# Performance work log

Measured on AMD Instinct MI355X. Metric: run time of the kernel, lower is better.

## Reference

```python
import jax, jax.numpy as jnp
import numpy as np

N = 100_000        # nodes
E = 3_200_000      # edges (avg degree 32)
F_IN = 2000        # highly-variable genes
H = 16             # hidden dim
C = 3              # KMeans clusters / classes


def setup_inputs() -> dict:
    key = jax.random.key(0)
    k1, k2, k3, k4 = jax.random.split(key, 4)
    x = jax.random.normal(k1, (N, F_IN), dtype=jnp.float32)
    edge_index = jax.random.randint(k2, (2, E), 0, N, dtype=jnp.int32)
    W1 = jax.random.normal(k3, (F_IN, H), dtype=jnp.float32) * (1.0 / np.sqrt(F_IN))
    b1 = jnp.zeros((H,), dtype=jnp.float32)
    W2 = jax.random.normal(k4, (H, C), dtype=jnp.float32) * (1.0 / np.sqrt(H))
    b2 = jnp.zeros((C,), dtype=jnp.float32)
    return {"x": x, "edge_index": edge_index, "W1": W1, "b1": b1, "W2": W2, "b2": b2}


def _gcn_conv(x, W, b, src, dst, n):
    """PyG GCNConv: linear -> add self-loops -> sym-normalized scatter-add -> +bias."""
    h = x @ W                                   # [N, F_out]
    loop = jnp.arange(n, dtype=src.dtype)
    src_sl = jnp.concatenate([src, loop])       # [E+N]
    dst_sl = jnp.concatenate([dst, loop])
    deg = jax.ops.segment_sum(jnp.ones(src_sl.shape[0], dtype=h.dtype), dst_sl, num_segments=n)
    dinv = jax.lax.rsqrt(deg)                   # deg >= 1 due to self-loops
    norm = dinv[src_sl] * dinv[dst_sl]          # [E+N]
    msg = h[src_sl] * norm[:, None]             # gather + scale
    out = jax.ops.segment_sum(msg, dst_sl, num_segments=n)  # scatter-add
    return out + b


def reference(x, edge_index, W1, b1, W2, b2):
    src, dst = edge_index[0], edge_index[1]
    n = x.shape[0]
    h = jax.nn.relu(_gcn_conv(x, W1, b1, src, dst, n))
    # F.dropout with training=False is identity (eval mode)
    logits = _gcn_conv(h, W2, b2, src, dst, n)
    return jax.nn.log_softmax(logits, axis=1)
```

## Files before the change

kernel.cpp:

```cpp
#include <hip/hip_runtime.h>
#include <hip/hip_bf16.h>


#define FIN   2000
#define HDIM  16
#define KB    40
#define NCHUNK (FIN / KB)
#define KSTRIDE 65

__global__ void zero_k(int4* __restrict__ p, int n4) {
    int i = blockIdx.x * 256 + threadIdx.x;
    if (i < n4) p[i] = make_int4(0, 0, 0, 0);
}

__global__ void count_k(const int* __restrict__ dst, int* __restrict__ cnt, int e) {
    int i = (blockIdx.x * 256 + threadIdx.x) * 4;
    if (i + 3 < e) {
        int4 d = *(const int4*)(dst + i);
        atomicAdd(&cnt[d.x], 1);
        atomicAdd(&cnt[d.y], 1);
        atomicAdd(&cnt[d.z], 1);
        atomicAdd(&cnt[d.w], 1);
    } else {
        for (int k = i; k < e; ++k) atomicAdd(&cnt[dst[k]], 1);
    }
}

__global__ __launch_bounds__(1024) void scan_k(const int* __restrict__ cnt,
                                               int* __restrict__ rowptr,
                                               float* __restrict__ dinv, int n) {
    __shared__ int sdata[1024];
    int tid = threadIdx.x;
    int chunk = (n + 1023) >> 10;
    int s0 = tid * chunk;
    int s1 = s0 + chunk; if (s1 > n) s1 = n;
    int sum = 0;
    for (int i = s0; i < s1; ++i) {
        int c = cnt[i];
        dinv[i] = 1.0f / sqrtf((float)(c + 1));
        sum += c;
    }
    sdata[tid] = sum;
    __syncthreads();
    for (int off = 1; off < 1024; off <<= 1) {
        int v = sdata[tid];
        int u = (tid >= off) ? sdata[tid - off] : 0;
        __syncthreads();
        sdata[tid] = v + u;
        __syncthreads();
    }
    int run = sdata[tid] - sum;
    for (int i = s0; i < s1; ++i) { rowptr[i] = run; run += cnt[i]; }
    if (tid == 0) rowptr[n] = sdata[1023];
}

__global__ void scatter_k(const int* __restrict__ src, const int* __restrict__ dst,
                          const int* __restrict__ rowptr, int* __restrict__ cursor,
                          int* __restrict__ col, int e) {
    int i = (blockIdx.x * 256 + threadIdx.x) * 4;
    if (i + 3 < e) {
        int4 d = *(const int4*)(dst + i);
        int4 s = *(const int4*)(src + i);
        col[rowptr[d.x] + atomicAdd(&cursor[d.x], 1)] = s.x;
        col[rowptr[d.y] + atomicAdd(&cursor[d.y], 1)] = s.y;
        col[rowptr[d.z] + atomicAdd(&cursor[d.z], 1)] = s.z;
        col[rowptr[d.w] + atomicAdd(&cursor[d.w], 1)] = s.w;
    } else {
        for (int k = i; k < e; ++k) {
            int d = dst[k];
            col[rowptr[d] + atomicAdd(&cursor[d], 1)] = src[k];
        }
    }
}

__global__ __launch_bounds__(64) void gemm1(const float* __restrict__ x,
                                            const float* __restrict__ W1,
                                            const float* __restrict__ dinv,
                                            float* __restrict__ t1s, int n) {
    __shared__ float xT[2][KB * KSTRIDE];
    const int lane = threadIdx.x;
    const long base = (long)blockIdx.x * 64;

    float4 st[10];

#define STAGE_LOAD(c)                                                       \
    {                                                                       \
        _Pragma("unroll")                                                   \
        for (int i = 0; i < 10; ++i) {                                      \
            int job = i * 64 + lane;                                        \
            int jr = job / 10, jk = job - jr * 10;                          \
            long gr = base + jr; if (gr >= n) gr = n - 1;                   \
            st[i] = *(const float4*)(x + gr * FIN + (c) * KB + jk * 4);     \
        }                                                                   \
    }
#define STAGE_WRITE(bsel)                                                   \
    {                                                                       \
        float* p = &xT[(bsel)][0];                                          \
        _Pragma("unroll")                                                   \
        for (int i = 0; i < 10; ++i) {                                      \
            int job = i * 64 + lane;                                        \
            int jr = job / 10, jk = job - jr * 10;                          \
            p[(jk * 4 + 0) * KSTRIDE + jr] = st[i].x;                       \
            p[(jk * 4 + 1) * KSTRIDE + jr] = st[i].y;                       \
            p[(jk * 4 + 2) * KSTRIDE + jr] = st[i].z;                       \
            p[(jk * 4 + 3) * KSTRIDE + jr] = st[i].w;                       \
        }                                                                   \
    }

    float acc[HDIM];
#pragma unroll
    for (int j = 0; j < HDIM; ++j) acc[j] = 0.0f;

    STAGE_LOAD(0);
    STAGE_WRITE(0);

    for (int c = 0; c < NCHUNK; ++c) {
        int b = c & 1;
        if (c + 1 < NCHUNK) STAGE_LOAD(c + 1);
        const float* w0 = W1 + c * KB * HDIM;
#pragma unroll 4
        for (int k = 0; k < KB; ++k) {
            float xv = xT[b][k * KSTRIDE + lane];
            const float* w = w0 + k * HDIM;
#pragma unroll
            for (int j = 0; j < HDIM; ++j) acc[j] = fmaf(xv, w[j], acc[j]);
        }
        if (c + 1 < NCHUNK) STAGE_WRITE((c + 1) & 1);
    }

    long row = base + lane;
    long rc = row < n ? row : n - 1;
    float s = dinv[rc];
    if (row < n) {
        float4* o = (float4*)(t1s + row * HDIM);
        o[0] = make_float4(acc[0] * s, acc[1] * s, acc[2] * s, acc[3] * s);
        o[1] = make_float4(acc[4] * s, acc[5] * s, acc[6] * s, acc[7] * s);
        o[2] = make_float4(acc[8] * s, acc[9] * s, acc[10] * s, acc[11] * s);
        o[3] = make_float4(acc[12] * s, acc[13] * s, acc[14] * s, acc[15] * s);
    }
#undef STAGE_LOAD
#undef STAGE_WRITE
}

__global__ __launch_bounds__(256) void agg1(const float* __restrict__ t1s,
                                            const int* __restrict__ rowptr,
                                            const int* __restrict__ col,
                                            const float* __restrict__ dinv,
                                            const float* __restrict__ b1,
                                            const float* __restrict__ W2,
                                            float* __restrict__ t2s, int n) {
    int node = blockIdx.x * 4 + (threadIdx.x >> 6);
    if (node >= n) return;
    int lane = threadIdx.x & 63;
    int nb = lane >> 4;
    int j  = lane & 15;
    int e0 = rowptr[node], e1 = rowptr[node + 1];
    float acc = (nb == 0) ? t1s[node * HDIM + j] : 0.0f;
    for (int e = e0 + nb; e < e1; e += 4) {
        acc += t1s[col[e] * HDIM + j];
    }
    acc += __shfl_xor(acc, 16);
    acc += __shfl_xor(acc, 32);
    float dn = dinv[node];
    float h = acc * dn + b1[j];
    h = h > 0.0f ? h : 0.0f;
    float p0 = h * W2[j * 3 + 0];
    float p1 = h * W2[j * 3 + 1];
    float p2 = h * W2[j * 3 + 2];
#pragma unroll
    for (int off = 8; off > 0; off >>= 1) {
        p0 += __shfl_xor(p0, off, 16);
        p1 += __shfl_xor(p1, off, 16);
        p2 += __shfl_xor(p2, off, 16);
    }
    if (lane == 0) {
        *(float4*)(t2s + node * 4) = make_float4(p0 * dn, p1 * dn, p2 * dn, 0.0f);
    }
}

__global__ __launch_bounds__(256) void agg2(const float* __restrict__ t2s,
                                            const int* __restrict__ rowptr,
                                            const int* __restrict__ col,
                                            const float* __restrict__ dinv,
                                            const float* __restrict__ b2,
                                            float* __restrict__ out, int n) {
    int node = blockIdx.x * 256 + threadIdx.x;
    if (node >= n) return;
    float4 a = *(const float4*)(t2s + node * 4);
    float a0 = a.x, a1 = a.y, a2 = a.z;
    int e0 = rowptr[node], e1 = rowptr[node + 1];
#pragma unroll 4
    for (int e = e0; e < e1; ++e) {
        int s = col[e];
        float4 v = *(const float4*)(t2s + s * 4);
        a0 += v.x; a1 += v.y; a2 += v.z;
    }
    float dn = dinv[node];
    float l0 = a0 * dn + b2[0];
    float l1 = a1 * dn + b2[1];
    float l2 = a2 * dn + b2[2];
    float m = fmaxf(l0, fmaxf(l1, l2));
    float lse = logf(expf(l0 - m) + expf(l1 - m) + expf(l2 - m)) + m;
    out[node * 3 + 0] = l0 - lse;
    out[node * 3 + 1] = l1 - lse;
    out[node * 3 + 2] = l2 - lse;
}

extern "C" void kernel_launch(void* const* d_in, const int* in_sizes, int n_in,
                              void* d_out, int out_size, void* d_ws, size_t ws_size,
                              hipStream_t stream) {
    const float* x  = (const float*)d_in[0];
    const int*   ei = (const int*)d_in[1];
    const float* W1 = (const float*)d_in[2];
    const float* b1 = (const float*)d_in[3];
    const float* W2 = (const float*)d_in[4];
    const float* b2 = (const float*)d_in[5];
    const int N = in_sizes[0] / FIN;
    const int E = in_sizes[1] / 2;
    const int* src = ei;
    const int* dst = ei + E;

    char* ws = (char*)d_ws;
    auto alloc = [&](size_t bytes) {
        char* p = ws;
        ws += (bytes + 255) & ~(size_t)255;
        return p;
    };
    size_t npad = ((size_t)N * 4 + 255) & ~(size_t)255;
    int*   cnt    = (int*)alloc(N * 4);
    int*   cursor = (int*)alloc(N * 4);
    int*   rowptr = (int*)alloc((size_t)(N + 1) * 4);
    float* dinv   = (float*)alloc(N * 4);
    int*   col    = (int*)alloc((size_t)E * 4);
    float* t1s    = (float*)alloc((size_t)N * HDIM * 4);
    float* t2s    = (float*)alloc((size_t)N * 4 * 4);

    int n4 = (int)(npad * 2 / 16);
    zero_k<<<(n4 + 255) / 256, 256, 0, stream>>>((int4*)cnt, n4);
    int e4 = (E + 3) / 4;
    count_k<<<(e4 + 255) / 256, 256, 0, stream>>>(dst, cnt, E);
    scan_k<<<1, 1024, 0, stream>>>(cnt, rowptr, dinv, N);
    scatter_k<<<(e4 + 255) / 256, 256, 0, stream>>>(src, dst, rowptr, cursor, col, E);
    gemm1<<<(N + 63) / 64, 64, 0, stream>>>(x, W1, dinv, t1s, N);
    agg1<<<(N + 3) / 4, 256, 0, stream>>>(t1s, rowptr, col, dinv, b1, W2, t2s, N);
    agg2<<<(N + 255) / 256, 256, 0, stream>>>(t2s, rowptr, col, dinv, b2, (float*)d_out, N);
}
```

Before: 857.7 us.

## Co-schedule split GEMM with edge count and CSR scatter in fused launches

The dense x@W1 GEMM is split into two halves. Each half runs in the same launch as one of the atomic-heavy graph-build passes: degree counting, and the CSR column scatter. Because dinv is not yet known when the first GEMM half runs, the GEMM now stores unscaled features, and agg1 multiplies each gathered neighbour row by dinv[src]. agg1 is also remapped to 16 lanes per node with a serial edge loop instead of 4 edge-parallel groups. The aim is to hide the latency-bound atomic passes behind the bandwidth-bound GEMM, at the cost of an extra dinv gather per edge and less edge-level parallelism in aggregation.

Result: no change. 867.3 us (+1.1%).

```diff
diff --git a/kernel.cpp b/kernel.cpp
--- a/kernel.cpp
+++ b/kernel.cpp
@@ -7,22 +7,140 @@
 #define KB    40
 #define NCHUNK (FIN / KB)
 #define KSTRIDE 65
+#define EPB   1024
 
 __global__ void zero_k(int4* __restrict__ p, int n4) {
     int i = blockIdx.x * 256 + threadIdx.x;
     if (i < n4) p[i] = make_int4(0, 0, 0, 0);
 }
 
-__global__ void count_k(const int* __restrict__ dst, int* __restrict__ cnt, int e) {
-    int i = (blockIdx.x * 256 + threadIdx.x) * 4;
-    if (i + 3 < e) {
-        int4 d = *(const int4*)(dst + i);
-        atomicAdd(&cnt[d.x], 1);
-        atomicAdd(&cnt[d.y], 1);
-        atomicAdd(&cnt[d.z], 1);
-        atomicAdd(&cnt[d.w], 1);
+__device__ __forceinline__ void gemm_body(const float* __restrict__ x,
+                                          const float* __restrict__ W1,
+                                          float* __restrict__ t1,
+                                          float xT[2][KB * KSTRIDE],
+                                          long base, int n) {
+    const int lane = threadIdx.x;
+    float4 st[10];
+
+#define STAGE_LOAD(c)                                                       \
+    {                                                                       \
+        _Pragma("unroll")                                                   \
+        for (int i = 0; i < 10; ++i) {                                      \
+            int job = i * 64 + lane;                                        \
+            int jr = job / 10, jk = job - jr * 10;                          \
+            long gr = base + jr; if (gr >= n) gr = n - 1;                   \
+            st[i] = *(const float4*)(x + gr * FIN + (c) * KB + jk * 4);     \
+        }                                                                   \
+    }
+#define STAGE_WRITE(bsel)                                                   \
+    {                                                                       \
+        float* p = &xT[(bsel)][0];                                          \
+        _Pragma("unroll")                                                   \
+        for (int i = 0; i < 10; ++i) {                                      \
+            int job = i * 64 + lane;                                        \
+            int jr = job / 10, jk = job - jr * 10;                          \
+            p[(jk * 4 + 0) * KSTRIDE + jr] = st[i].x;                       \
+            p[(jk * 4 + 1) * KSTRIDE + jr] = st[i].y;                       \
+            p[(jk * 4 + 2) * KSTRIDE + jr] = st[i].z;                       \
+            p[(jk * 4 + 3) * KSTRIDE + jr] = st[i].w;                       \
+        }                                                                   \
+    }
+
+    float acc[HDIM];
+#pragma unroll
+    for (int j = 0; j < HDIM; ++j) acc[j] = 0.0f;
+
+    STAGE_LOAD(0);
+    STAGE_WRITE(0);
+
+    for (int c = 0; c < NCHUNK; ++c) {
+        int b = c & 1;
+        if (c + 1 < NCHUNK) STAGE_LOAD(c + 1);
+        const float* w0 = W1 + c * KB * HDIM;
+        __syncthreads();
+#pragma unroll 4
+        for (int k = 0; k < KB; ++k) {
+            float xv = xT[b][k * KSTRIDE + lane];
+            const float* w = w0 + k * HDIM;
+#pragma unroll
+            for (int j = 0; j < HDIM; ++j) acc[j] = fmaf(xv, w[j], acc[j]);
+        }
+        __syncthreads();
+        if (c + 1 < NCHUNK) STAGE_WRITE((c + 1) & 1);
+    }
+
+    long row = base + lane;
+    if (row < n) {
+        float4* o = (float4*)(t1 + row * HDIM);
+        o[0] = make_float4(acc[0], acc[1], acc[2], acc[3]);
+        o[1] = make_float4(acc[4], acc[5], acc[6], acc[7]);
+        o[2] = make_float4(acc[8], acc[9], acc[10], acc[11]);
+        o[3] = make_float4(acc[12], acc[13], acc[14], acc[15]);
+    }
+#undef STAGE_LOAD
+#undef STAGE_WRITE
+}
+
+__global__ __launch_bounds__(64) void fused_a(const float* __restrict__ x,
+                                              const float* __restrict__ W1,
+                                              float* __restrict__ t1,
+                                              const int* __restrict__ dst,
+                                              int* __restrict__ cnt,
+                                              int n, int e, int ga) {
+    __shared__ float xT[2][KB * KSTRIDE];
+    if ((int)blockIdx.x < ga) {
+        gemm_body(x, W1, t1, xT, (long)blockIdx.x * 64, n);
     } else {
-        for (int k = i; k < e; ++k) atomicAdd(&cnt[dst[k]], 1);
+        int chunk = blockIdx.x - ga;
+        int base = chunk * EPB + (int)threadIdx.x * 4;
+#pragma unroll
+        for (int r = 0; r < 4; ++r) {
+            int i = base + r * 256;
+            if (i + 3 < e) {
+                int4 d = *(const int4*)(dst + i);
+                atomicAdd(&cnt[d.x], 1);
+                atomicAdd(&cnt[d.y], 1);
+                atomicAdd(&cnt[d.z], 1);
+                atomicAdd(&cnt[d.w], 1);
+            } else {
+                for (int k = i; k < e && k < i + 4; ++k) atomicAdd(&cnt[dst[k]], 1);
+            }
+        }
+    }
+}
+
+__global__ __launch_bounds__(64) void fused_b(const float* __restrict__ x,
+                                              const float* __restrict__ W1,
+                                              float* __restrict__ t1,
+                                              const int* __restrict__ src,
+                                              const int* __restrict__ dst,
+                                              const int* __restrict__ rowptr,
+                                              int* __restrict__ cursor,
+                                              int* __restrict__ col,
+                                              int n, int e, int ga, int gb) {
+    __shared__ float xT[2][KB * KSTRIDE];
+    if ((int)blockIdx.x < gb) {
+        gemm_body(x, W1, t1, xT, (long)(ga + blockIdx.x) * 64, n);
+    } else {
+        int chunk = blockIdx.x - gb;
+        int base = chunk * EPB + (int)threadIdx.x * 4;
+#pragma unroll
+        for (int r = 0; r < 4; ++r) {
+            int i = base + r * 256;
+            if (i + 3 < e) {
+                int4 d = *(const int4*)(dst + i);
+                int4 s = *(const int4*)(src + i);
+                col[rowptr[d.x] + atomicAdd(&cursor[d.x], 1)] = s.x;
+                col[rowptr[d.y] + atomicAdd(&cursor[d.y], 1)] = s.y;
+                col[rowptr[d.z] + atomicAdd(&cursor[d.z], 1)] = s.z;
+                col[rowptr[d.w] + atomicAdd(&cursor[d.w], 1)] = s.w;
+            } else {
+                for (int k = i; k < e && k < i + 4; ++k) {
+                    int d = dst[k];
+                    col[rowptr[d] + atomicAdd(&cursor[d], 1)] = src[k];
+                }
+            }
+        }
     }
 }
 
@@ -54,114 +172,24 @@
     if (tid == 0) rowptr[n] = sdata[1023];
 }
 
-__global__ void scatter_k(const int* __restrict__ src, const int* __restrict__ dst,
-                          const int* __restrict__ rowptr, int* __restrict__ cursor,
-                          int* __restrict__ col, int e) {
-    int i = (blockIdx.x * 256 + threadIdx.x) * 4;
-    if (i + 3 < e) {
-        int4 d = *(const int4*)(dst + i);
-        int4 s = *(const int4*)(src + i);
-        col[rowptr[d.x] + atomicAdd(&cursor[d.x], 1)] = s.x;
-        col[rowptr[d.y] + atomicAdd(&cursor[d.y], 1)] = s.y;
-        col[rowptr[d.z] + atomicAdd(&cursor[d.z], 1)] = s.z;
-        col[rowptr[d.w] + atomicAdd(&cursor[d.w], 1)] = s.w;
-    } else {
-        for (int k = i; k < e; ++k) {
-            int d = dst[k];
-            col[rowptr[d] + atomicAdd(&cursor[d], 1)] = src[k];
-        }
-    }
-}
-
-__global__ __launch_bounds__(64) void gemm1(const float* __restrict__ x,
-                                            const float* __restrict__ W1,
-                                            const float* __restrict__ dinv,
-                                            float* __restrict__ t1s, int n) {
-    __shared__ float xT[2][KB * KSTRIDE];
-    const int lane = threadIdx.x;
-    const long base = (long)blockIdx.x * 64;
-
-    float4 st[10];
-
-#define STAGE_LOAD(c)                                                       \
-    {                                                                       \
-        _Pragma("unroll")                                                   \
-        for (int i = 0; i < 10; ++i) {                                      \
-            int job = i * 64 + lane;                                        \
-            int jr = job / 10, jk = job - jr * 10;                          \
-            long gr = base + jr; if (gr >= n) gr = n - 1;                   \
-            st[i] = *(const float4*)(x + gr * FIN + (c) * KB + jk * 4);     \
-        }                                                                   \
-    }
-#define STAGE_WRITE(bsel)                                                   \
-    {                                                                       \
-        float* p = &xT[(bsel)][0];                                          \
-        _Pragma("unroll")                                                   \
-        for (int i = 0; i < 10; ++i) {                                      \
-            int job = i * 64 + lane;                                        \
-            int jr = job / 10, jk = job - jr * 10;                          \
-            p[(jk * 4 + 0) * KSTRIDE + jr] = st[i].x;                       \
-            p[(jk * 4 + 1) * KSTRIDE + jr] = st[i].y;                       \
-            p[(jk * 4 + 2) * KSTRIDE + jr] = st[i].z;                       \
-            p[(jk * 4 + 3) * KSTRIDE + jr] = st[i].w;                       \
-        }                                                                   \
-    }
-
-    float acc[HDIM];
-#pragma unroll
-    for (int j = 0; j < HDIM; ++j) acc[j] = 0.0f;
-
-    STAGE_LOAD(0);
-    STAGE_WRITE(0);
-
-    for (int c = 0; c < NCHUNK; ++c) {
-        int b = c & 1;
-        if (c + 1 < NCHUNK) STAGE_LOAD(c + 1);
-        const float* w0 = W1 + c * KB * HDIM;
-#pragma unroll 4
-        for (int k = 0; k < KB; ++k) {
-            float xv = xT[b][k * KSTRIDE + lane];
-            const float* w = w0 + k * HDIM;
-#pragma unroll
-            for (int j = 0; j < HDIM; ++j) acc[j] = fmaf(xv, w[j], acc[j]);
-        }
-        if (c + 1 < NCHUNK) STAGE_WRITE((c + 1) & 1);
-    }
-
-    long row = base + lane;
-    long rc = row < n ? row : n - 1;
-    float s = dinv[rc];
-    if (row < n) {
-        float4* o = (float4*)(t1s + row * HDIM);
-        o[0] = make_float4(acc[0] * s, acc[1] * s, acc[2] * s, acc[3] * s);
-        o[1] = make_float4(acc[4] * s, acc[5] * s, acc[6] * s, acc[7] * s);
-        o[2] = make_float4(acc[8] * s, acc[9] * s, acc[10] * s, acc[11] * s);
-        o[3] = make_float4(acc[12] * s, acc[13] * s, acc[14] * s, acc[15] * s);
-    }
-#undef STAGE_LOAD
-#undef STAGE_WRITE
-}
-
-__global__ __launch_bounds__(256) void agg1(const float* __restrict__ t1s,
+__global__ __launch_bounds__(256) void agg1(const float* __restrict__ t1,
                                             const int* __restrict__ rowptr,
                                             const int* __restrict__ col,
                                             const float* __restrict__ dinv,
                                             const float* __restrict__ b1,
                                             const float* __restrict__ W2,
                                             float* __restrict__ t2s, int n) {
-    int node = blockIdx.x * 4 + (threadIdx.x >> 6);
+    int tid = blockIdx.x * 256 + threadIdx.x;
+    int node = tid >> 4;
+    int j = tid & 15;
     if (node >= n) return;
-    int lane = threadIdx.x & 63;
-    int nb = lane >> 4;
-    int j  = lane & 15;
+    float dn = dinv[node];
+    float acc = t1[node * HDIM + j] * dn;
     int e0 = rowptr[node], e1 = rowptr[node + 1];
-    float acc = (nb == 0) ? t1s[node * HDIM + j] : 0.0f;
-    for (int e = e0 + nb; e < e1; e += 4) {
-        acc += t1s[col[e] * HDIM + j];
-    }
-    acc += __shfl_xor(acc, 16);
-    acc += __shfl_xor(acc, 32);
-    float dn = dinv[node];
+    for (int e = e0; e < e1; ++e) {
+        int s = col[e];
+        acc += t1[s * HDIM + j] * dinv[s];
+    }
     float h = acc * dn + b1[j];
     h = h > 0.0f ? h : 0.0f;
     float p0 = h * W2[j * 3 + 0];
@@ -173,7 +201,7 @@
         p1 += __shfl_xor(p1, off, 16);
         p2 += __shfl_xor(p2, off, 16);
     }
-    if (lane == 0) {
+    if (j == 0) {
         *(float4*)(t2s + node * 4) = make_float4(p0 * dn, p1 * dn, p2 * dn, 0.0f);
     }
 }
@@ -232,16 +260,21 @@
     int*   rowptr = (int*)alloc((size_t)(N + 1) * 4);
     float* dinv   = (float*)alloc(N * 4);
     int*   col    = (int*)alloc((size_t)E * 4);
-    float* t1s    = (float*)alloc((size_t)N * HDIM * 4);
+    float* t1     = (float*)alloc((size_t)N * HDIM * 4);
     float* t2s    = (float*)alloc((size_t)N * 4 * 4);
 
     int n4 = (int)(npad * 2 / 16);
     zero_k<<<(n4 + 255) / 256, 256, 0, stream>>>((int4*)cnt, n4);
-    int e4 = (E + 3) / 4;
-    count_k<<<(e4 + 255) / 256, 256, 0, stream>>>(dst, cnt, E);
+
+    int gemm_blocks = (N + 63) / 64;
+    int ga = (gemm_blocks + 1) / 2;
+    int gb = gemm_blocks - ga;
+    int light = (E + EPB - 1) / EPB;
+
+    fused_a<<<ga + light, 64, 0, stream>>>(x, W1, t1, dst, cnt, N, E, ga);
     scan_k<<<1, 1024, 0, stream>>>(cnt, rowptr, dinv, N);
-    scatter_k<<<(e4 + 255) / 256, 256, 0, stream>>>(src, dst, rowptr, cursor, col, E);
-    gemm1<<<(N + 63) / 64, 64, 0, stream>>>(x, W1, dinv, t1s, N);
-    agg1<<<(N + 3) / 4, 256, 0, stream>>>(t1s, rowptr, col, dinv, b1, W2, t2s, N);
+    fused_b<<<gb + light, 64, 0, stream>>>(x, W1, t1, src, dst, rowptr, cursor, col,
+                                           N, E, ga, gb);
+    agg1<<<(N * 16 + 255) / 256, 256, 0, stream>>>(t1, rowptr, col, dinv, b1, W2, t2s, N);
     agg2<<<(N + 255) / 256, 256, 0, stream>>>(t2s, rowptr, col, dinv, b2, (float*)d_out, N);
 }
```

## Split GEMM output columns across half-waves and use one 16-lane group per node in agg1

Applied to the files above, without the earlier changes.

The first GEMM now covers 32 rows per 64-thread block, with each half-wave computing 8 of the 16 output columns. This doubles the block count and halves the per-thread accumulator and staging registers, aiming at more parallelism and occupancy on the bandwidth-bound x stream. The first aggregation now gives each node a single 16-lane group that walks all its edges serially, instead of four neighbour streams per node merged by cross-lane shuffles. That removes the shuffle reduction and packs four nodes per wave, but lengthens the serial gather loop per node.

New measurement: 1.123 ms. +30.9%, slower.

```diff
diff --git a/kernel.cpp b/kernel.cpp
--- a/kernel.cpp
+++ b/kernel.cpp
@@ -6,7 +6,9 @@
 #define HDIM  16
 #define KB    40
 #define NCHUNK (FIN / KB)
-#define KSTRIDE 65
+#define RW    32
+#define KST   33
+#define NF4   5
 
 __global__ void zero_k(int4* __restrict__ p, int n4) {
     int i = blockIdx.x * 256 + threadIdx.x;
@@ -77,16 +79,18 @@
                                             const float* __restrict__ W1,
                                             const float* __restrict__ dinv,
                                             float* __restrict__ t1s, int n) {
-    __shared__ float xT[2][KB * KSTRIDE];
+    __shared__ float xT[2][KB * KST];
     const int lane = threadIdx.x;
-    const long base = (long)blockIdx.x * 64;
-
-    float4 st[10];
+    const int r    = lane & 31;
+    const int half = lane >> 5;
+    const long base = (long)blockIdx.x * RW;
+
+    float4 st[NF4];
 
 #define STAGE_LOAD(c)                                                       \
     {                                                                       \
         _Pragma("unroll")                                                   \
-        for (int i = 0; i < 10; ++i) {                                      \
+        for (int i = 0; i < NF4; ++i) {                                     \
             int job = i * 64 + lane;                                        \
             int jr = job / 10, jk = job - jr * 10;                          \
             long gr = base + jr; if (gr >= n) gr = n - 1;                   \
@@ -97,19 +101,19 @@
     {                                                                       \
         float* p = &xT[(bsel)][0];                                          \
         _Pragma("unroll")                                                   \
-        for (int i = 0; i < 10; ++i) {                                      \
+        for (int i = 0; i < NF4; ++i) {                                     \
             int job = i * 64 + lane;                                        \
             int jr = job / 10, jk = job - jr * 10;                          \
-            p[(jk * 4 + 0) * KSTRIDE + jr] = st[i].x;                       \
-            p[(jk * 4 + 1) * KSTRIDE + jr] = st[i].y;                       \
-            p[(jk * 4 + 2) * KSTRIDE + jr] = st[i].z;                       \
-            p[(jk * 4 + 3) * KSTRIDE + jr] = st[i].w;                       \
+            p[(jk * 4 + 0) * KST + jr] = st[i].x;                           \
+            p[(jk * 4 + 1) * KST + jr] = st[i].y;                           \
+            p[(jk * 4 + 2) * KST + jr] = st[i].z;                           \
+            p[(jk * 4 + 3) * KST + jr] = st[i].w;                           \
         }                                                                   \
     }
 
-    float acc[HDIM];
+    float acc[8];
 #pragma unroll
-    for (int j = 0; j < HDIM; ++j) acc[j] = 0.0f;
+    for (int u = 0; u < 8; ++u) acc[u] = 0.0f;
 
     STAGE_LOAD(0);
     STAGE_WRITE(0);
@@ -117,26 +121,23 @@
     for (int c = 0; c < NCHUNK; ++c) {
         int b = c & 1;
         if (c + 1 < NCHUNK) STAGE_LOAD(c + 1);
-        const float* w0 = W1 + c * KB * HDIM;
+        const float* w0 = W1 + c * KB * HDIM + half * 8;
 #pragma unroll 4
         for (int k = 0; k < KB; ++k) {
-            float xv = xT[b][k * KSTRIDE + lane];
+            float xv = xT[b][k * KST + r];
             const float* w = w0 + k * HDIM;
 #pragma unroll
-            for (int j = 0; j < HDIM; ++j) acc[j] = fmaf(xv, w[j], acc[j]);
+            for (int u = 0; u < 8; ++u) acc[u] = fmaf(xv, w[u], acc[u]);
         }
         if (c + 1 < NCHUNK) STAGE_WRITE((c + 1) & 1);
     }
 
-    long row = base + lane;
-    long rc = row < n ? row : n - 1;
-    float s = dinv[rc];
+    long row = base + r;
     if (row < n) {
-        float4* o = (float4*)(t1s + row * HDIM);
-        o[0] = make_float4(acc[0] * s, acc[1] * s, acc[2] * s, acc[3] * s);
-        o[1] = make_float4(acc[4] * s, acc[5] * s, acc[6] * s, acc[7] * s);
-        o[2] = make_float4(acc[8] * s, acc[9] * s, acc[10] * s, acc[11] * s);
-        o[3] = make_float4(acc[12] * s, acc[13] * s, acc[14] * s, acc[15] * s);
+        float sc = dinv[row];
+        float4* o = (float4*)(t1s + row * HDIM + half * 8);
+        o[0] = make_float4(acc[0] * sc, acc[1] * sc, acc[2] * sc, acc[3] * sc);
+        o[1] = make_float4(acc[4] * sc, acc[5] * sc, acc[6] * sc, acc[7] * sc);
     }
 #undef STAGE_LOAD
 #undef STAGE_WRITE
@@ -149,18 +150,16 @@
                                             const float* __restrict__ b1,
                                             const float* __restrict__ W2,
                                             float* __restrict__ t2s, int n) {
-    int node = blockIdx.x * 4 + (threadIdx.x >> 6);
+    int tid = blockIdx.x * 256 + threadIdx.x;
+    int node = tid >> 4;
+    int j = tid & 15;
     if (node >= n) return;
-    int lane = threadIdx.x & 63;
-    int nb = lane >> 4;
-    int j  = lane & 15;
+    float acc = t1s[node * HDIM + j];
     int e0 = rowptr[node], e1 = rowptr[node + 1];
-    float acc = (nb == 0) ? t1s[node * HDIM + j] : 0.0f;
-    for (int e = e0 + nb; e < e1; e += 4) {
-        acc += t1s[col[e] * HDIM + j];
-    }
-    acc += __shfl_xor(acc, 16);
-    acc += __shfl_xor(acc, 32);
+    for (int e = e0; e < e1; ++e) {
+        int s = col[e];
+        acc += t1s[s * HDIM + j];
+    }
     float dn = dinv[node];
     float h = acc * dn + b1[j];
     h = h > 0.0f ? h : 0.0f;
@@ -173,7 +172,7 @@
         p1 += __shfl_xor(p1, off, 16);
         p2 += __shfl_xor(p2, off, 16);
     }
-    if (lane == 0) {
+    if (j == 0) {
         *(float4*)(t2s + node * 4) = make_float4(p0 * dn, p1 * dn, p2 * dn, 0.0f);
     }
 }
@@ -241,7 +240,7 @@
     count_k<<<(e4 + 255) / 256, 256, 0, stream>>>(dst, cnt, E);
     scan_k<<<1, 1024, 0, stream>>>(cnt, rowptr, dinv, N);
     scatter_k<<<(e4 + 255) / 256, 256, 0, stream>>>(src, dst, rowptr, cursor, col, E);
-    gemm1<<<(N + 63) / 64, 64, 0, stream>>>(x, W1, dinv, t1s, N);
-    agg1<<<(N + 3) / 4, 256, 0, stream>>>(t1s, rowptr, col, dinv, b1, W2, t2s, N);
+    gemm1<<<(N + RW - 1) / RW, 64, 0, stream>>>(x, W1, dinv, t1s, N);
+    agg1<<<(N * 16 + 255) / 256, 256, 0, stream>>>(t1s, rowptr, col, dinv, b1, W2, t2s, N);
     agg2<<<(N + 255) / 256, 256, 0, stream>>>(t2s, rowptr, col, dinv, b2, (float*)d_out, N);
 }
```
